# Kernel optimization log

Measured on AMD Instinct MI355X. Metric: run time of the kernel, lower is better.

Reference implementation:

```python
import jax, jax.numpy as jnp
import numpy as np

ISIZE = 1024
OSIZE = 1024
EPS = 1e-5  # torch nn.LayerNorm default


def setup_inputs() -> dict:
    key = jax.random.key(0)
    k0, k1, k2 = jax.random.split(key, 3)
    B, S = 32, 256
    x = jax.random.normal(k0, (B, S, ISIZE), dtype=jnp.float32)
    # Linear(isize + osize, 4*osize): W stored as (in, out) for x @ W
    scale = 1.0 / np.sqrt(ISIZE + OSIZE)
    W = jax.random.uniform(k1, (ISIZE + OSIZE, 4 * OSIZE), dtype=jnp.float32,
                           minval=-scale, maxval=scale)
    b = jax.random.uniform(k2, (4 * OSIZE,), dtype=jnp.float32,
                           minval=-scale, maxval=scale)
    gamma = jnp.ones((4, OSIZE), dtype=jnp.float32)   # LayerNorm((4, osize)) weight
    beta = jnp.zeros((4, OSIZE), dtype=jnp.float32)   # LayerNorm((4, osize)) bias
    init_hx = jnp.zeros((1, OSIZE), dtype=jnp.float32)
    init_cx = jnp.zeros((1, OSIZE), dtype=jnp.float32)
    return {"x": x, "W": W, "b": b, "gamma": gamma, "beta": beta,
            "init_hx": init_hx, "init_cx": init_cx}


def _layernorm_2d(z, gamma, beta):
    # Normalize jointly over the last two dims (4, osize), per torch LayerNorm((4, osize))
    mean = jnp.mean(z, axis=(-2, -1), keepdims=True)
    var = jnp.var(z, axis=(-2, -1), keepdims=True)
    return (z - mean) * jax.lax.rsqrt(var + EPS) * gamma + beta


def reference(x, W, b, gamma, beta, init_hx, init_cx):
    B, S, _ = x.shape
    osize = init_hx.shape[-1]
    hx = jnp.broadcast_to(init_hx, (B, osize))  # prepare_initState: expand to batch
    cx = jnp.broadcast_to(init_cx, (B, osize))

    def step(carry, xt):
        h, c = carry
        comb = jnp.concatenate([xt, h], axis=-1) @ W + b       # [B, 4*osize]
        comb = _layernorm_2d(comb.reshape(B, 4, osize), gamma, beta)
        ig, fg, hidden, og = comb[:, 0], comb[:, 1], comb[:, 2], comb[:, 3]
        c = jax.nn.sigmoid(fg) * c + jax.nn.sigmoid(ig) * jnp.tanh(hidden)
        h = jax.nn.sigmoid(og) * c                              # RNMT+ cell: out = og * cell
        return (h, c), h

    xs = jnp.swapaxes(x, 0, 1)                                  # [S, B, isize]
    _, outs = jax.lax.scan(step, (hx, cx), xs)
    return jnp.swapaxes(outs, 0, 1)                             # [B, S, osize]
```

## Files before the change

### kernel.cpp

```cpp
#include <hip/hip_runtime.h>
#include <hip/hip_bf16.h>

#define NB 32
#define NS 256
#define NI 1024
#define NO 1024
#define NK 2048
#define NC 4096
#define LN_EPS 1e-5f

typedef __attribute__((ext_vector_type(4))) float f32x4;
typedef __attribute__((ext_vector_type(4))) unsigned int u32x4;

__device__ __forceinline__ f32x4 mfma_bf16_16x16x32(u32x4 a, u32x4 b, f32x4 c) {
  asm volatile("v_mfma_f32_16x16x32_bf16 %0, %1, %2, %0" : "+v"(c) : "v"(a), "v"(b));
  return c;
}

__device__ __forceinline__ float sigf(float x) { return 1.0f / (1.0f + __expf(-x)); }
__device__ __forceinline__ float tanhfast(float x) {
  return 1.0f - 2.0f / (__expf(2.0f * x) + 1.0f);
}


__global__ void pack_x(const float* __restrict__ x, __hip_bfloat16* __restrict__ xfrag) {
  const int t = blockIdx.x, kt = blockIdx.y;
  const int tid = threadIdx.x;
  const int plane = tid >> 6, l = tid & 63, q = (l >> 4), ln = l & 15;
  const int m = plane * 16 + ln;
  const float* src = x + ((size_t)m * NS + t) * NI + kt * 32 + q * 8;
  float4 v0 = *(const float4*)src;
  float4 v1 = *(const float4*)(src + 4);
  __align__(16) __hip_bfloat16 tmp[8];
  tmp[0] = __float2bfloat16(v0.x); tmp[1] = __float2bfloat16(v0.y);
  tmp[2] = __float2bfloat16(v0.z); tmp[3] = __float2bfloat16(v0.w);
  tmp[4] = __float2bfloat16(v1.x); tmp[5] = __float2bfloat16(v1.y);
  tmp[6] = __float2bfloat16(v1.z); tmp[7] = __float2bfloat16(v1.w);
  *(u32x4*)(xfrag + (((size_t)t * 32 + kt) * 2 + plane) * 512 + l * 8) = *(const u32x4*)tmp;
}

__global__ void pack_wf(const float* __restrict__ W, __hip_bfloat16* __restrict__ WF) {
  const int blk = blockIdx.x;
  const int b = blk >> 6, kt = blk & 63;
  const int l = threadIdx.x, q = l >> 4, c = l & 15;
  const int n  = ((c >> 2) << 10) + b * 4 + (c & 3);
  const int k0 = kt * 32 + q * 8;
  __align__(16) __hip_bfloat16 tmp[8];
#pragma unroll
  for (int j = 0; j < 8; ++j)
    tmp[j] = __float2bfloat16(W[(size_t)(k0 + j) * NC + n]);
  *(u32x4*)(WF + ((size_t)(b * 64 + kt) * 64 + l) * 8) = *(const u32x4*)tmp;
}

__device__ __forceinline__ size_t hfrag_idx(int m, int j) {
  const int kt = j >> 5, q = (j >> 3) & 3, jj = j & 7;
  const int plane = m >> 4, l = q * 16 + (m & 15);
  return (((size_t)kt * 2 + plane) * 64 + l) * 8 + jj;
}

__global__ void init_state(const float* __restrict__ hx0, const float* __restrict__ cx0,
                           __hip_bfloat16* __restrict__ hfrag, float* __restrict__ cst,
                           float* __restrict__ hf) {
  const int i = blockIdx.x * 256 + threadIdx.x;
  const int m = i >> 10, j = i & (NO - 1);
  const float hv = hx0[j];
  hfrag[hfrag_idx(m, j)] = __float2bfloat16(hv);
  hf[i]  = hv;
  cst[i] = cx0[j];
}

__global__ __launch_bounds__(512)
void step_gemm_mfma(const __hip_bfloat16* __restrict__ xfrag,
                    const __hip_bfloat16* __restrict__ hfrag,
                    const __hip_bfloat16* __restrict__ WF,
                    const float* __restrict__ bias,
                    float* __restrict__ comb, int t) {
  __shared__ __align__(16) float xch[8 * 2 * 256];
  const int b = blockIdx.x, tid = threadIdx.x;
  const int wv = tid >> 6, l = tid & 63;

  const __hip_bfloat16* ap = (wv < 4)
      ? xfrag + ((size_t)t * 32 + wv * 8) * 1024 + l * 8
      : hfrag + ((size_t)(wv - 4) * 8) * 1024 + l * 8;
  const __hip_bfloat16* bp = WF + ((size_t)(b * 64 + wv * 8) * 64 + l) * 8;

  f32x4 acc0 = {0.f, 0.f, 0.f, 0.f}, acc1 = {0.f, 0.f, 0.f, 0.f};
  asm volatile("s_nop 1" ::);
#pragma unroll
  for (int i = 0; i < 8; ++i) {
    u32x4 a0 = *(const u32x4*)(ap + (size_t)i * 1024);
    u32x4 a1 = *(const u32x4*)(ap + (size_t)i * 1024 + 512);
    u32x4 bb = *(const u32x4*)(bp + (size_t)i * 512);
    acc0 = mfma_bf16_16x16x32(a0, bb, acc0);
    acc1 = mfma_bf16_16x16x32(a1, bb, acc1);
  }
  asm volatile("s_nop 7\n\ts_nop 7" ::);

  *(f32x4*)(xch + (wv * 2 + 0) * 256 + l * 4) = acc0;
  *(f32x4*)(xch + (wv * 2 + 1) * 256 + l * 4) = acc1;
  __syncthreads();

  const int row = tid >> 4, c = tid & 15;
  const int p = row >> 4, rr = row & 15;
  const int idx = ((rr >> 2) * 16 + c) * 4 + (rr & 3);
  const int n = ((c >> 2) << 10) + b * 4 + (c & 3);
  float v = bias[n];
#pragma unroll
  for (int w = 0; w < 8; ++w) v += xch[(w * 2 + p) * 256 + idx];
  comb[(size_t)row * NC + n] = v;
}

__global__ __launch_bounds__(1024)
void step_update_row(const float* __restrict__ comb,
                     const float* __restrict__ gamma,
                     const float* __restrict__ beta,
                     float* __restrict__ cst,
                     float* __restrict__ out,
                     __hip_bfloat16* __restrict__ hfrag,
                     int t) {
  __shared__ __align__(16) float combL[NC];
  __shared__ float red[16][2];
  __shared__ float stat[2];
  const int m = blockIdx.x, tid = threadIdx.x;

  f32x4 cv = *(const f32x4*)(comb + (size_t)m * NC + tid * 4);
  *(f32x4*)(combL + tid * 4) = cv;
  float s  = cv[0] + cv[1] + cv[2] + cv[3];
  float ss = cv[0] * cv[0] + cv[1] * cv[1] + cv[2] * cv[2] + cv[3] * cv[3];
#pragma unroll
  for (int off = 1; off < 64; off <<= 1) {
    s  += __shfl_xor(s, off);
    ss += __shfl_xor(ss, off);
  }
  const int wid = tid >> 6;
  if ((tid & 63) == 0) { red[wid][0] = s; red[wid][1] = ss; }
  __syncthreads();
  if (tid == 0) {
    float s2 = 0.f, ss2 = 0.f;
#pragma unroll
    for (int i = 0; i < 16; ++i) { s2 += red[i][0]; ss2 += red[i][1]; }
    const float mean = s2 * (1.f / NC);
    const float var  = ss2 * (1.f / NC) - mean * mean;
    stat[0] = mean;
    stat[1] = rsqrtf(var + LN_EPS);
  }
  __syncthreads();
  const float mean = stat[0], rs = stat[1];
  const int j = tid;
  const float iv = (combL[j]          - mean) * rs * gamma[j]          + beta[j];
  const float fv = (combL[NO + j]     - mean) * rs * gamma[NO + j]     + beta[NO + j];
  const float gv = (combL[2 * NO + j] - mean) * rs * gamma[2 * NO + j] + beta[2 * NO + j];
  const float ov = (combL[3 * NO + j] - mean) * rs * gamma[3 * NO + j] + beta[3 * NO + j];
  const float cold = cst[(size_t)m * NO + j];
  const float cc = sigf(fv) * cold + sigf(iv) * tanhfast(gv);
  const float hh = sigf(ov) * cc;
  cst[(size_t)m * NO + j] = cc;
  out[((size_t)m * NS + t) * NO + j] = hh;
  hfrag[hfrag_idx(m, j)] = __float2bfloat16(hh);
}


__launch_bounds__(256)
__global__ void step_gemm_f32(const float* __restrict__ x, const float* __restrict__ hf,
                              const float* __restrict__ W, const float* __restrict__ bias,
                              float* __restrict__ comb, int t) {
  const int blk = blockIdx.x;
  const int tid = threadIdx.x;
  const int n   = blk * 16 + (tid & 15);
  const int mlo = tid >> 4;
  float a0 = 0.f, a1 = 0.f;
  for (int k = 0; k < NI; ++k) {
    const float wv = W[(size_t)k * NC + n];
    a0 += x[((size_t)mlo * NS + t) * NI + k] * wv;
    a1 += x[((size_t)(mlo + 16) * NS + t) * NI + k] * wv;
  }
  for (int k = 0; k < NO; ++k) {
    const float wv = W[(size_t)(NI + k) * NC + n];
    a0 += hf[mlo * NO + k] * wv;
    a1 += hf[(mlo + 16) * NO + k] * wv;
  }
  comb[(size_t)mlo * NC + n] = a0 + bias[n];
  comb[(size_t)(mlo + 16) * NC + n] = a1 + bias[n];
}

__global__ __launch_bounds__(1024)
void step_update_row_f32(const float* __restrict__ comb,
                         const float* __restrict__ gamma,
                         const float* __restrict__ beta,
                         float* __restrict__ cst,
                         float* __restrict__ out,
                         float* __restrict__ hf,
                         int t) {
  __shared__ __align__(16) float combL[NC];
  __shared__ float red[16][2];
  __shared__ float stat[2];
  const int m = blockIdx.x, tid = threadIdx.x;
  f32x4 cv = *(const f32x4*)(comb + (size_t)m * NC + tid * 4);
  *(f32x4*)(combL + tid * 4) = cv;
  float s  = cv[0] + cv[1] + cv[2] + cv[3];
  float ss = cv[0] * cv[0] + cv[1] * cv[1] + cv[2] * cv[2] + cv[3] * cv[3];
#pragma unroll
  for (int off = 1; off < 64; off <<= 1) {
    s  += __shfl_xor(s, off);
    ss += __shfl_xor(ss, off);
  }
  const int wid = tid >> 6;
  if ((tid & 63) == 0) { red[wid][0] = s; red[wid][1] = ss; }
  __syncthreads();
  if (tid == 0) {
    float s2 = 0.f, ss2 = 0.f;
    for (int i = 0; i < 16; ++i) { s2 += red[i][0]; ss2 += red[i][1]; }
    const float mean = s2 * (1.f / NC);
    const float var  = ss2 * (1.f / NC) - mean * mean;
    stat[0] = mean;
    stat[1] = rsqrtf(var + LN_EPS);
  }
  __syncthreads();
  const float mean = stat[0], rs = stat[1];
  const int j = tid;
  const float iv = (combL[j]          - mean) * rs * gamma[j]          + beta[j];
  const float fv = (combL[NO + j]     - mean) * rs * gamma[NO + j]     + beta[NO + j];
  const float gv = (combL[2 * NO + j] - mean) * rs * gamma[2 * NO + j] + beta[2 * NO + j];
  const float ov = (combL[3 * NO + j] - mean) * rs * gamma[3 * NO + j] + beta[3 * NO + j];
  const float cold = cst[(size_t)m * NO + j];
  const float cc = sigf(fv) * cold + sigf(iv) * tanhfast(gv);
  const float hh = sigf(ov) * cc;
  cst[(size_t)m * NO + j] = cc;
  out[((size_t)m * NS + t) * NO + j] = hh;
  hf[(size_t)m * NO + j] = hh;
}


extern "C" void kernel_launch(void* const* d_in, const int* in_sizes, int n_in,
                              void* d_out, int out_size, void* d_ws, size_t ws_size,
                              hipStream_t stream) {
  (void)in_sizes; (void)n_in; (void)out_size;
  const float* x     = (const float*)d_in[0];
  const float* W     = (const float*)d_in[1];
  const float* bias  = (const float*)d_in[2];
  const float* gamma = (const float*)d_in[3];
  const float* beta  = (const float*)d_in[4];
  const float* hx0   = (const float*)d_in[5];
  const float* cx0   = (const float*)d_in[6];
  float* outp = (float*)d_out;

  char* ws = (char*)d_ws;
  size_t off = 0;
  auto alloc = [&](size_t bytes) -> char* {
    off = (off + 255) & ~(size_t)255;
    char* p = ws + off;
    off += bytes;
    return p;
  };
  float* comb          = (float*)alloc((size_t)NB * NC * 4);
  float* cst           = (float*)alloc((size_t)NB * NO * 4);
  float* hf            = (float*)alloc((size_t)NB * NO * 4);
  __hip_bfloat16* hfrag = (__hip_bfloat16*)alloc((size_t)NB * NO * 2);
  __hip_bfloat16* xfrag = (__hip_bfloat16*)alloc((size_t)NB * NS * NI * 2);
  __hip_bfloat16* WF    = (__hip_bfloat16*)alloc((size_t)NK * NC * 2);
  const bool big = (ws_size >= off);

  hipLaunchKernelGGL(init_state, dim3((NB * NO) / 256), dim3(256), 0, stream,
                     hx0, cx0, hfrag, cst, hf);
  if (big) {
    hipLaunchKernelGGL(pack_x, dim3(NS, 32), dim3(128), 0, stream, x, xfrag);
    hipLaunchKernelGGL(pack_wf, dim3(256 * 64), dim3(64), 0, stream, W, WF);
    for (int t = 0; t < NS; ++t) {
      hipLaunchKernelGGL(step_gemm_mfma, dim3(256), dim3(512), 0, stream,
                         xfrag, hfrag, WF, bias, comb, t);
      hipLaunchKernelGGL(step_update_row, dim3(NB), dim3(1024), 0, stream,
                         comb, gamma, beta, cst, outp, hfrag, t);
    }
  } else {
    for (int t = 0; t < NS; ++t) {
      hipLaunchKernelGGL(step_gemm_f32, dim3(256), dim3(256), 0, stream,
                         x, hf, W, bias, comb, t);
      hipLaunchKernelGGL(step_update_row_f32, dim3(NB), dim3(1024), 0, stream,
                         comb, gamma, beta, cst, outp, hf, t);
    }
  }
}
```

Measured before the change: 2.446 ms.

## Hoist input projection x@W_x out of recurrence into one batched GEMM

Adds a precompute_xw kernel that computes the input contribution x_t@W_x plus bias for all 256 timesteps in one large batched MFMA GEMM before the time loop. Each per-step GEMM then only multiplies the hidden state by the recurrent half of W and adds the precomputed row. This halves the K dimension of the serial per-step work and moves the rest into a highly parallel kernel. The cost is a 128 MB fp32 workspace buffer, which is read back every step. A tiered fallback keeps the old path when the workspace is too small.

New measurement: 2.506 ms. 1.02x slower.

```diff
diff --git a/kernel.cpp b/kernel.cpp
--- a/kernel.cpp
+++ b/kernel.cpp
@@ -67,6 +67,96 @@
   hfrag[hfrag_idx(m, j)] = __float2bfloat16(hv);
   hf[i]  = hv;
   cst[i] = cx0[j];
+}
+
+__global__ __launch_bounds__(512)
+void precompute_xw(const __hip_bfloat16* __restrict__ xfrag,
+                   const __hip_bfloat16* __restrict__ WF,
+                   const float* __restrict__ bias,
+                   float* __restrict__ xw) {
+  const int tq = blockIdx.x, nb = blockIdx.y;
+  const int tid = threadIdx.x;
+  const int w = tid >> 6, l = tid & 63, q = l >> 4, c = l & 15;
+  const int tp = w >> 2, ng = w & 3;
+  const int t0  = tq * 4 + tp * 2;
+  const int bg0 = nb * 8 + ng * 2;
+
+  float bias_g[2];
+#pragma unroll
+  for (int g = 0; g < 2; ++g)
+    bias_g[g] = bias[((c >> 2) << 10) + (bg0 + g) * 4 + (c & 3)];
+
+  f32x4 acc[2][2][2] = {};
+  asm volatile("s_nop 1" ::);
+  for (int kt = 0; kt < 32; ++kt) {
+    u32x4 a[2][2], bb[2];
+#pragma unroll
+    for (int tt = 0; tt < 2; ++tt)
+#pragma unroll
+      for (int p = 0; p < 2; ++p)
+        a[tt][p] = *(const u32x4*)(xfrag +
+            (((size_t)(t0 + tt) * 32 + kt) * 2 + p) * 512 + l * 8);
+#pragma unroll
+    for (int g = 0; g < 2; ++g)
+      bb[g] = *(const u32x4*)(WF + (((size_t)(bg0 + g) * 64 + kt) * 64 + l) * 8);
+#pragma unroll
+    for (int tt = 0; tt < 2; ++tt)
+#pragma unroll
+      for (int p = 0; p < 2; ++p)
+#pragma unroll
+        for (int g = 0; g < 2; ++g)
+          acc[tt][p][g] = mfma_bf16_16x16x32(a[tt][p], bb[g], acc[tt][p][g]);
+  }
+  asm volatile("s_nop 7\n\ts_nop 7" ::);
+#pragma unroll
+  for (int tt = 0; tt < 2; ++tt)
+#pragma unroll
+    for (int p = 0; p < 2; ++p)
+#pragma unroll
+      for (int g = 0; g < 2; ++g) {
+        const int n = ((c >> 2) << 10) + (bg0 + g) * 4 + (c & 3);
+#pragma unroll
+        for (int r = 0; r < 4; ++r) {
+          const int row = p * 16 + q * 4 + r;
+          xw[((size_t)(t0 + tt) * 32 + row) * NC + n] = acc[tt][p][g][r] + bias_g[g];
+        }
+      }
+}
+
+__global__ __launch_bounds__(512)
+void step_gemm_h(const __hip_bfloat16* __restrict__ hfrag,
+                 const __hip_bfloat16* __restrict__ WF,
+                 const float* __restrict__ xw,
+                 float* __restrict__ comb, int t) {
+  __shared__ __align__(16) float xch[8 * 256];
+  const int b = blockIdx.x, tid = threadIdx.x;
+  const int w = tid >> 6, l = tid & 63;
+  const int p = w & 1, k0 = (w >> 1) * 8;
+
+  const __hip_bfloat16* ap = hfrag + ((size_t)k0 * 2 + p) * 512 + l * 8;
+  const __hip_bfloat16* bp = WF + (((size_t)b * 64 + 32 + k0) * 64 + l) * 8;
+
+  f32x4 acc = {0.f, 0.f, 0.f, 0.f};
+  asm volatile("s_nop 1" ::);
+#pragma unroll
+  for (int i = 0; i < 8; ++i) {
+    u32x4 a  = *(const u32x4*)(ap + (size_t)i * 1024);
+    u32x4 bb = *(const u32x4*)(bp + (size_t)i * 512);
+    acc = mfma_bf16_16x16x32(a, bb, acc);
+  }
+  asm volatile("s_nop 7\n\ts_nop 7" ::);
+
+  *(f32x4*)(xch + w * 256 + l * 4) = acc;
+  __syncthreads();
+
+  const int row = tid >> 4, c = tid & 15;
+  const int pp = row >> 4, rr = row & 15;
+  const int idx = ((rr >> 2) * 16 + c) * 4 + (rr & 3);
+  const int n = ((c >> 2) << 10) + b * 4 + (c & 3);
+  float v = xw[((size_t)t * 32 + row) * NC + n];
+#pragma unroll
+  for (int i = 0; i < 4; ++i) v += xch[(i * 2 + pp) * 256 + idx];
+  comb[(size_t)row * NC + n] = v;
 }
 
 __global__ __launch_bounds__(512)
@@ -252,17 +342,31 @@
     off += bytes;
     return p;
   };
-  float* comb          = (float*)alloc((size_t)NB * NC * 4);
-  float* cst           = (float*)alloc((size_t)NB * NO * 4);
-  float* hf            = (float*)alloc((size_t)NB * NO * 4);
+  float* comb           = (float*)alloc((size_t)NB * NC * 4);
+  float* cst            = (float*)alloc((size_t)NB * NO * 4);
+  float* hf             = (float*)alloc((size_t)NB * NO * 4);
   __hip_bfloat16* hfrag = (__hip_bfloat16*)alloc((size_t)NB * NO * 2);
   __hip_bfloat16* xfrag = (__hip_bfloat16*)alloc((size_t)NB * NS * NI * 2);
   __hip_bfloat16* WF    = (__hip_bfloat16*)alloc((size_t)NK * NC * 2);
-  const bool big = (ws_size >= off);
+  const size_t off_mid = off;
+  float* xw             = (float*)alloc((size_t)NS * NB * NC * 4);
+  const size_t off_full = off;
+  const int tier = (ws_size >= off_full) ? 2 : (ws_size >= off_mid) ? 1 : 0;
 
   hipLaunchKernelGGL(init_state, dim3((NB * NO) / 256), dim3(256), 0, stream,
                      hx0, cx0, hfrag, cst, hf);
-  if (big) {
+  if (tier == 2) {
+    hipLaunchKernelGGL(pack_x, dim3(NS, 32), dim3(128), 0, stream, x, xfrag);
+    hipLaunchKernelGGL(pack_wf, dim3(256 * 64), dim3(64), 0, stream, W, WF);
+    hipLaunchKernelGGL(precompute_xw, dim3(64, 32), dim3(512), 0, stream,
+                       xfrag, WF, bias, xw);
+    for (int t = 0; t < NS; ++t) {
+      hipLaunchKernelGGL(step_gemm_h, dim3(256), dim3(512), 0, stream,
+                         hfrag, WF, xw, comb, t);
+      hipLaunchKernelGGL(step_update_row, dim3(NB), dim3(1024), 0, stream,
+                         comb, gamma, beta, cst, outp, hfrag, t);
+    }
+  } else if (tier == 1) {
     hipLaunchKernelGGL(pack_x, dim3(NS, 32), dim3(128), 0, stream, x, xfrag);
     hipLaunchKernelGGL(pack_wf, dim3(256 * 64), dim3(64), 0, stream, W, WF);
     for (int t = 0; t < NS; ++t) {
```
